# Performance work log

Hardware: AMD Instinct MI355X
Metric: run time of the kernel (lower is better)

The kernel has to match this reference:

```python
import jax, jax.numpy as jnp
import numpy as np


def setup_inputs() -> dict:
    key = jax.random.key(0)
    ks = jax.random.split(key, 5)
    N, C, H, W = 4, 256, 64, 64
    E, O = 256, 256  # embed_channels, out_channels
    scale = 1.0 / np.sqrt(C)
    return {
        "x": jax.random.normal(ks[0], (N, C, H, W), dtype=jnp.float32),
        "Wq": jax.random.normal(ks[1], (E, C), dtype=jnp.float32) * scale,
        "bq": jax.random.normal(ks[2], (E,), dtype=jnp.float32) * 0.01,
        "Wkv": jax.random.normal(ks[3], (E + O, C), dtype=jnp.float32) * scale,
        "bkv": jax.random.normal(ks[4], (E + O,), dtype=jnp.float32) * 0.01,
    }


def reference(x, Wq, bq, Wkv, bkv):
    n, c, h, w = x.shape
    E = Wq.shape[0]
    S = h * w
    # 1x1 convs == per-pixel linear projections over channels.
    # q: [n, S, E] (row-major hw flatten matches torch .view(n, C, -1))
    q = (jnp.einsum('nchw,ec->nhwe', x, Wq) + bq).reshape(n, S, E)
    kv = jnp.einsum('nchw,oc->nhwo', x, Wkv) + bkv  # [n, h, w, E+O]
    k = kv[..., :E].reshape(n, S, E)
    v = kv[..., E:].reshape(n, S, -1)  # [n, S, O]
    O = v.shape[-1]
    # Causal mask: tril with diagonal=0 (pixel may attend to itself and earlier).
    mask = jnp.tril(jnp.ones((S, S), dtype=bool))
    attn = jnp.einsum('nse,nte->nst', q, k) / np.sqrt(E)  # [n, S, S]
    attn = jnp.where(mask, attn, -jnp.inf)
    attn = jax.nn.softmax(attn, axis=-1)
    out = jnp.einsum('nst,nto->nso', attn, v)  # [n, S, O]
    return jnp.transpose(out, (0, 2, 1)).reshape(n, O, h, w)
```

## Files before the change

kernel.cpp:

```cpp
#include <hip/hip_runtime.h>
#include <hip/hip_bf16.h>

typedef __bf16 bf16x8 __attribute__((ext_vector_type(8)));
typedef float f32x4 __attribute__((ext_vector_type(4)));
typedef short short8 __attribute__((ext_vector_type(8)));
typedef short short4v __attribute__((ext_vector_type(4)));

#define NB 4
#define CC 256
#define SS 4096
#define EE 256

static constexpr float QSCALE = 1.4426950408889634f / 16.0f;

#define QOFF 0u
#define KOFF 8388608u
#define VOFF 16777216u
#define WOFF 25165824u
#define BOFF 25559040u
#define PAOFF 25690112u

#define GLOAD_LDS16(gsrc, ldst) \
    __builtin_amdgcn_global_load_lds((const __attribute__((address_space(1))) void*)(gsrc), \
                                     (__attribute__((address_space(3))) void*)(ldst), 16, 0, 0)

__global__ __launch_bounds__(256) void prep_kernel(const float* __restrict__ Wq,
                                                   const float* __restrict__ bq,
                                                   const float* __restrict__ Wkv,
                                                   const float* __restrict__ bkv,
                                                   __bf16* __restrict__ wc,
                                                   float* __restrict__ bias) {
    int r = blockIdx.x;
    int t = threadIdx.x;
    float v;
    if (r < 256) v = Wq[r * 256 + t] * QSCALE;
    else         v = Wkv[(r - 256) * 256 + t];
    wc[r * 256 + t] = (__bf16)v;
    if (t == 0) bias[r] = (r < 256) ? bq[r] * QSCALE : bkv[r - 256];
}

__global__ __launch_bounds__(256) void proj_kernel(const float* __restrict__ x,
                                                   const __bf16* __restrict__ wc,
                                                   const float* __restrict__ bias,
                                                   __bf16* __restrict__ qo,
                                                   __bf16* __restrict__ ko,
                                                   __bf16* __restrict__ vo) {
    __shared__ __align__(16) char Ab[32768];
    __shared__ __align__(16) char Wb[32768];
    const int t = threadIdx.x;
    const int lane = t & 63;
    const int w = t >> 6;
    const int n = blockIdx.x >> 6;
    const int s0 = (blockIdx.x & 63) << 6;

    {
        const int sl = t & 15;
        const int cc0 = t >> 4;
        #pragma unroll
        for (int it = 0; it < 2; ++it) {
            int c0 = (cc0 + (it << 4)) << 3;
            float f[8][4];
            #pragma unroll
            for (int r = 0; r < 8; ++r) {
                const float* xp = x + ((long)(n * CC + c0 + r)) * SS + s0 + sl;
                #pragma unroll
                for (int i = 0; i < 4; ++i) f[r][i] = xp[i << 4];
            }
            #pragma unroll
            for (int i = 0; i < 4; ++i) {
                bf16x8 v;
                #pragma unroll
                for (int r = 0; r < 8; ++r) v[r] = (__bf16)f[r][i];
                int srow = sl + (i << 4);
                *(bf16x8*)(Ab + srow * 512 + ((c0 * 2) ^ ((srow & 7) << 4))) = v;
            }
        }
    }
    __syncthreads();

    bf16x8 af[8];
    {
        int arow = (w << 4) + (lane & 15);
        #pragma unroll
        for (int kf = 0; kf < 8; ++kf) {
            int c = ((lane >> 4) << 3) + (kf << 5);
            af[kf] = *(const bf16x8*)(Ab + arow * 512 + ((c * 2) ^ ((arow & 7) << 4)));
        }
    }

    for (int ot = 0; ot < 12; ++ot) {
        #pragma unroll
        for (int p = 0; p < 16; ++p) {
            int row = w + (p << 2);
            int c = lane << 2;
            short4v vv = *(const short4v*)((const short*)wc + (ot * 64 + row) * 256 + c);
            *(short4v*)(Wb + row * 512 + ((c * 2) ^ ((row & 7) << 4))) = vv;
        }
        __syncthreads();

        f32x4 acc[4];
        #pragma unroll
        for (int cb = 0; cb < 4; ++cb) acc[cb] = (f32x4){0.f, 0.f, 0.f, 0.f};
        #pragma unroll
        for (int cb = 0; cb < 4; ++cb) {
            int row = (cb << 4) + (lane & 15);
            #pragma unroll
            for (int kf = 0; kf < 8; ++kf) {
                int c = ((lane >> 4) << 3) + (kf << 5);
                bf16x8 bfr = *(const bf16x8*)(Wb + row * 512 + ((c * 2) ^ ((row & 7) << 4)));
                acc[cb] = __builtin_amdgcn_mfma_f32_16x16x32_bf16(af[kf], bfr, acc[cb], 0, 0, 0);
            }
        }
        __syncthreads();

        __bf16* T = (__bf16*)Wb;
        float bsv[4];
        #pragma unroll
        for (int cb = 0; cb < 4; ++cb) bsv[cb] = bias[ot * 64 + (cb << 4) + (lane & 15)];

        if (ot < 8) {
            #pragma unroll
            for (int cb = 0; cb < 4; ++cb) {
                #pragma unroll
                for (int jj = 0; jj < 4; ++jj) {
                    int srow = (w << 4) + ((lane >> 4) << 2) + jj;
                    T[srow * 72 + (cb << 4) + (lane & 15)] = (__bf16)(acc[cb][jj] + bsv[cb]);
                }
            }
            __syncthreads();
            int s = t >> 2;
            int o0 = (t & 3) << 4;
            short8 r0 = *(const short8*)((const short*)T + s * 72 + o0);
            short8 r1 = *(const short8*)((const short*)T + s * 72 + o0 + 8);
            __bf16* dst = (ot < 4) ? qo : ko;
            long idx = ((long)(n * SS + s0 + s)) * EE + ((ot & 3) << 6) + o0;
            *(short8*)((short*)dst + idx) = r0;
            *(short8*)((short*)dst + idx + 8) = r1;
        } else {
            #pragma unroll
            for (int cb = 0; cb < 4; ++cb) {
                #pragma unroll
                for (int jj = 0; jj < 4; ++jj) {
                    int srow = (w << 4) + ((lane >> 4) << 2) + jj;
                    T[((cb << 4) + (lane & 15)) * 72 + srow] = (__bf16)(acc[cb][jj] + bsv[cb]);
                }
            }
            __syncthreads();
            int o = t >> 2;
            int sc0 = (t & 3) << 4;
            short8 r0 = *(const short8*)((const short*)T + o * 72 + sc0);
            short8 r1 = *(const short8*)((const short*)T + o * 72 + sc0 + 8);
            long idx = ((long)((n << 8) + ((ot - 8) << 6) + o)) * SS + s0 + sc0;
            *(short8*)((short*)vo + idx) = r0;
            *(short8*)((short*)vo + idx + 8) = r1;
        }
        __syncthreads();
    }
}

__global__ __launch_bounds__(512, 2) void attn_kernel(const __bf16* __restrict__ qg,
                                                      const __bf16* __restrict__ kg,
                                                      const __bf16* __restrict__ vg,
                                                      float* __restrict__ out,
                                                      float* __restrict__ pacc,
                                                      float2* __restrict__ pstats,
                                                      int chs, int ncs, int direct) {
    __shared__ __align__(16) char SMEM[147456];
    char* Pb = SMEM + 131072;
    const int t = threadIdx.x;
    const int lane = t & 63;
    const int w = t >> 6;

    const int b = blockIdx.x;
    const int c = b & ((1 << ncs) - 1);
    const int rest = b >> ncs;
    const int qtr = rest & 31;
    const int qt = 31 - qtr;
    const int n = rest >> 5;
    const int jtop = (qt << 1) + 1;
    const int jlo = c << chs;
    if (jlo > jtop) return;
    const int jhi = (jtop < jlo + (1 << chs) - 1) ? jtop : (jlo + (1 << chs) - 1);
    const int s0 = qt << 7;
    const int wr_direct = direct || ((jtop >> chs) == 0);

    auto stageK = [&](int j, int pb) {
        char* Kb = SMEM + (pb << 15);
        const int t0 = j << 6;
        #pragma unroll
        for (int i = 0; i < 4; ++i) {
            int rl = (i << 4) + (w << 1) + (lane >> 5);
            const short* src = (const short*)kg + ((long)(n * SS + t0 + rl)) * EE
                               + (((lane & 31) << 3) ^ ((rl & 7) << 3));
            GLOAD_LDS16(src, Kb + ((i << 4) + (w << 1)) * 512);
        }
    };
    auto stageV = [&](int j, int pb) {
        char* Vt = SMEM + 65536 + (pb << 15);
        const int t0 = j << 6;
        #pragma unroll
        for (int i = 0; i < 4; ++i) {
            int o = (i << 6) + (w << 3) + (lane >> 3);
            const short* src = (const short*)vg + ((long)((n << 8) + o)) * SS + t0
                               + (((lane & 7) << 3) ^ ((o & 7) << 3));
            GLOAD_LDS16(src, Vt + ((i << 6) + (w << 3)) * 128);
        }
    };

    bf16x8 qf[8];
    {
        int qrow = s0 + (w << 4) + (lane & 15);
        const short* qp = (const short*)qg + ((long)(n * SS + qrow)) * EE;
        #pragma unroll
        for (int kf = 0; kf < 8; ++kf)
            qf[kf] = *(const bf16x8*)(qp + ((lane >> 4) << 3) + (kf << 5));
    }

    float m_[4], ls[4];
    #pragma unroll
    for (int rr = 0; rr < 4; ++rr) { m_[rr] = -3e38f; ls[rr] = 0.f; }
    f32x4 acc[16];
    #pragma unroll
    for (int ocb = 0; ocb < 16; ++ocb) acc[ocb] = (f32x4){0.f, 0.f, 0.f, 0.f};

    stageK(jlo, jlo & 1);
    stageV(jlo, jlo & 1);

    for (int j = jlo; j <= jhi; ++j) {
        const int p = j & 1;
        const int t0 = j << 6;
        char* Kb = SMEM + (p << 15);
        char* Vt = SMEM + 65536 + (p << 15);
        __syncthreads();

        if (j < jhi) {
            stageK(j + 1, p ^ 1);
            stageV(j + 1, p ^ 1);
        }

        f32x4 sacc[4];
        #pragma unroll
        for (int cb = 0; cb < 4; ++cb) sacc[cb] = (f32x4){0.f, 0.f, 0.f, 0.f};
        #pragma unroll
        for (int cb = 0; cb < 4; ++cb) {
            int row = (cb << 4) + (lane & 15);
            #pragma unroll
            for (int kf = 0; kf < 8; ++kf) {
                int slot = (lane >> 4) + (kf << 2);
                bf16x8 kb = *(const bf16x8*)(Kb + row * 512 + ((slot ^ (row & 7)) << 4));
                sacc[cb] = __builtin_amdgcn_mfma_f32_16x16x32_bf16(qf[kf], kb, sacc[cb], 0, 0, 0);
            }
        }

        if ((j >> 1) == qt) {
            #pragma unroll
            for (int cb = 0; cb < 4; ++cb) {
                int key = t0 + (cb << 4) + (lane & 15);
                #pragma unroll
                for (int rr = 0; rr < 4; ++rr) {
                    int qr = s0 + (w << 4) + ((lane >> 4) << 2) + rr;
                    if (key > qr) sacc[cb][rr] = -1e30f;
                }
            }
        }

        float mx[4], ps[4], scl[4];
        #pragma unroll
        for (int rr = 0; rr < 4; ++rr)
            mx[rr] = fmaxf(fmaxf(sacc[0][rr], sacc[1][rr]), fmaxf(sacc[2][rr], sacc[3][rr]));
        #pragma unroll
        for (int off = 1; off < 16; off <<= 1) {
            #pragma unroll
            for (int rr = 0; rr < 4; ++rr) mx[rr] = fmaxf(mx[rr], __shfl_xor(mx[rr], off));
        }
        float pv[4][4];
        #pragma unroll
        for (int rr = 0; rr < 4; ++rr) {
            float mn = fmaxf(m_[rr], mx[rr]);
            scl[rr] = exp2f(m_[rr] - mn);
            m_[rr] = mn;
        }
        #pragma unroll
        for (int cb = 0; cb < 4; ++cb)
            #pragma unroll
            for (int rr = 0; rr < 4; ++rr) pv[cb][rr] = exp2f(sacc[cb][rr] - m_[rr]);
        #pragma unroll
        for (int rr = 0; rr < 4; ++rr)
            ps[rr] = (pv[0][rr] + pv[1][rr]) + (pv[2][rr] + pv[3][rr]);
        #pragma unroll
        for (int off = 1; off < 16; off <<= 1) {
            #pragma unroll
            for (int rr = 0; rr < 4; ++rr) ps[rr] += __shfl_xor(ps[rr], off);
        }
        #pragma unroll
        for (int rr = 0; rr < 4; ++rr) ls[rr] = ls[rr] * scl[rr] + ps[rr];

        #pragma unroll
        for (int cb = 0; cb < 4; ++cb)
            #pragma unroll
            for (int rr = 0; rr < 4; ++rr) {
                int row = ((lane >> 4) << 2) + rr;
                int col = (cb << 4) + (lane & 15);
                *(__bf16*)(Pb + (w << 11) + (row << 7)
                           + (((col >> 3) ^ (row & 7)) << 4) + ((col & 7) << 1)) = (__bf16)pv[cb][rr];
            }

        #pragma unroll
        for (int ocb = 0; ocb < 16; ++ocb)
            #pragma unroll
            for (int rr = 0; rr < 4; ++rr) acc[ocb][rr] *= scl[rr];

        bf16x8 pa[2];
        #pragma unroll
        for (int kf2 = 0; kf2 < 2; ++kf2) {
            int prow = lane & 15;
            int pslot = (lane >> 4) + (kf2 << 2);
            pa[kf2] = *(const bf16x8*)(Pb + (w << 11) + (prow << 7) + ((pslot ^ (prow & 7)) << 4));
        }
        #pragma unroll
        for (int ocb = 0; ocb < 16; ++ocb) {
            int orow = (ocb << 4) + (lane & 15);
            #pragma unroll
            for (int kf2 = 0; kf2 < 2; ++kf2) {
                int slot = (lane >> 4) + (kf2 << 2);
                bf16x8 vb = *(const bf16x8*)(Vt + (orow << 7) + ((slot ^ (orow & 7)) << 4));
                acc[ocb] = __builtin_amdgcn_mfma_f32_16x16x32_bf16(pa[kf2], vb, acc[ocb], 0, 0, 0);
            }
        }
    }

    if (!wr_direct && (lane & 15) == 0) {
        #pragma unroll
        for (int rr = 0; rr < 4; ++rr) {
            int s = (w << 4) + ((lane >> 4) << 2) + rr;
            pstats[(long)b * 128 + s] = make_float2(m_[rr], ls[rr]);
        }
    }

    float inv[4];
    #pragma unroll
    for (int rr = 0; rr < 4; ++rr) inv[rr] = wr_direct ? (1.0f / ls[rr]) : 1.0f;
    float* T = (float*)SMEM;

#define EPI_STAGE(g)                                                                    \
    do {                                                                                \
        __syncthreads();                                                                \
        _Pragma("unroll")                                                               \
        for (int e = 0; e < 2; ++e) {                                                   \
            _Pragma("unroll")                                                           \
            for (int rr = 0; rr < 4; ++rr) {                                            \
                int ol = (e << 4) + (lane & 15);                                        \
                int cl = (w << 4) + ((lane >> 4) << 2) + rr;                            \
                T[ol * 132 + cl] = acc[((g) << 1) + e][rr] * inv[rr];                   \
            }                                                                           \
        }                                                                               \
        __syncthreads();                                                                \
        {                                                                               \
            int row = t >> 4;                                                \
            int c0 = (t & 15) << 3;                               \
            float* dp = wr_direct                                                       \
                ? (out + ((long)((n << 8) + ((g) << 5) + row)) * SS + s0 + c0)          \
                : (pacc + ((long)b << 15) + ((((g) << 5) + row) << 7) + c0);            \
            f32x4 r0 = *(const f32x4*)(T + row * 132 + c0);                             \
            f32x4 r1 = *(const f32x4*)(T + row * 132 + c0 + 4);                         \
            *(f32x4*)dp = r0;                                                           \
            *(f32x4*)(dp + 4) = r1;                                                     \
        }                                                                               \
    } while (0)

    EPI_STAGE(0); EPI_STAGE(1); EPI_STAGE(2); EPI_STAGE(3);
    EPI_STAGE(4); EPI_STAGE(5); EPI_STAGE(6); EPI_STAGE(7);
#undef EPI_STAGE
}

__global__ __launch_bounds__(256) void combine_kernel(const float* __restrict__ pacc,
                                                      const float2* __restrict__ pstats,
                                                      float* __restrict__ out,
                                                      int chs, int ncs) {
    const int t = threadIdx.x;
    const int b2 = blockIdx.x;
    const int og = b2 & 7;
    const int qtr = (b2 >> 3) & 31;
    const int qt = 31 - qtr;
    const int n = b2 >> 8;
    const int jtop = (qt << 1) + 1;
    const int nch = (jtop >> chs) + 1;
    if (nch == 1) return;
    const long sb0 = (long)(((n << 5) + qtr) << ncs);

    __shared__ float wsc[8][128];
    __shared__ float invL[128];
    if (t < 128) {
        float M = -3e38f;
        for (int c2 = 0; c2 < nch; ++c2) M = fmaxf(M, pstats[(sb0 + c2) * 128 + t].x);
        float L = 0.f;
        for (int c2 = 0; c2 < nch; ++c2) {
            float2 st = pstats[(sb0 + c2) * 128 + t];
            float wv = exp2f(st.x - M);
            wsc[c2][t] = wv;
            L += st.y * wv;
        }
        invL[t] = 1.f / L;
    }
    __syncthreads();

    const int o = (og << 5) + (t >> 3);
    const int sc = (t & 7) << 4;
    float a[16];
    #pragma unroll
    for (int i = 0; i < 16; ++i) a[i] = 0.f;
    for (int c2 = 0; c2 < nch; ++c2) {
        const float* p = pacc + ((sb0 + c2) << 15) + (o << 7) + sc;
        #pragma unroll
        for (int u = 0; u < 4; ++u) {
            f32x4 v = *(const f32x4*)(p + (u << 2));
            #pragma unroll
            for (int k2 = 0; k2 < 4; ++k2) a[(u << 2) + k2] += v[k2] * wsc[c2][sc + (u << 2) + k2];
        }
    }
    float* op = out + ((long)((n << 8) + o)) * SS + (qt << 7) + sc;
    #pragma unroll
    for (int u = 0; u < 4; ++u) {
        f32x4 r;
        #pragma unroll
        for (int k2 = 0; k2 < 4; ++k2) r[k2] = a[(u << 2) + k2] * invL[sc + (u << 2) + k2];
        *(f32x4*)(op + (u << 2)) = r;
    }
}

extern "C" void kernel_launch(void* const* d_in, const int* in_sizes, int n_in,
                              void* d_out, int out_size, void* d_ws, size_t ws_size,
                              hipStream_t stream) {
    const float* x   = (const float*)d_in[0];
    const float* Wq  = (const float*)d_in[1];
    const float* bq  = (const float*)d_in[2];
    const float* Wkv = (const float*)d_in[3];
    const float* bkv = (const float*)d_in[4];
    float* out = (float*)d_out;
    char* ws = (char*)d_ws;
    __bf16* qw = (__bf16*)(ws + QOFF);
    __bf16* kw = (__bf16*)(ws + KOFF);
    __bf16* vw = (__bf16*)(ws + VOFF);
    __bf16* wc = (__bf16*)(ws + WOFF);
    float*  bias = (float*)(ws + BOFF);

    size_t need = (size_t)PAOFF + (size_t)1024 * 131072 + (size_t)1024 * 1024;
    int direct = (ws_size < need) ? 1 : 0;
    int ncs = direct ? 0 : 3;
    int chs = direct ? 6 : 3;
    float* pacc = (float*)(ws + PAOFF);
    float2* pstats = (float2*)(ws + PAOFF + (size_t)1024 * 131072);

    prep_kernel<<<dim3(768), dim3(256), 0, stream>>>(Wq, bq, Wkv, bkv, wc, bias);
    proj_kernel<<<dim3(256), dim3(256), 0, stream>>>(x, wc, bias, qw, kw, vw);
    attn_kernel<<<dim3(128 << ncs), dim3(512), 0, stream>>>(qw, kw, vw, out, pacc, pstats,
                                                            chs, ncs, direct);
    if (!direct)
        combine_kernel<<<dim3(1024), dim3(256), 0, stream>>>(pacc, pstats, out, chs, ncs);
}
```

Before: 199.1 us.

## Remap attention blocks to XCDs per batch and skip unneeded softmax rescales

Block IDs are remapped so that each pair of XCDs handles a single batch element, so its K/V tiles stay in that XCD's L2. The partial-output and stats slots are indexed to match the new mapping. Separately, the online softmax now keeps the running max unchanged when every row's new max exceeds it by at most 8 (log2 units), which skips the exp2 and the 64-register accumulator rescale on most iterations. The deferred max allows exponentials up to 2^8, a small overflow and precision risk in bf16 P. It also adds a wave-wide vote each iteration.

```diff
diff --git a/kernel.cpp b/kernel.cpp
--- a/kernel.cpp
+++ b/kernel.cpp
@@ -171,12 +171,13 @@
     const int lane = t & 63;
     const int w = t >> 6;
 
-    const int b = blockIdx.x;
-    const int c = b & ((1 << ncs) - 1);
-    const int rest = b >> ncs;
-    const int qtr = rest & 31;
+    const int xcd = blockIdx.x & 7;
+    const int n = xcd >> 1;
+    const int id = ((blockIdx.x >> 3) << 1) | (xcd & 1);
+    const int c = id & ((1 << ncs) - 1);
+    const int qtr = (id >> ncs) & 31;
     const int qt = 31 - qtr;
-    const int n = rest >> 5;
+    const long slot = ((long)n << (5 + ncs)) + id;
     const int jtop = (qt << 1) + 1;
     const int jlo = c << chs;
     if (jlo > jtop) return;
@@ -246,8 +247,8 @@
             int row = (cb << 4) + (lane & 15);
             #pragma unroll
             for (int kf = 0; kf < 8; ++kf) {
-                int slot = (lane >> 4) + (kf << 2);
-                bf16x8 kb = *(const bf16x8*)(Kb + row * 512 + ((slot ^ (row & 7)) << 4));
+                int slotk = (lane >> 4) + (kf << 2);
+                bf16x8 kb = *(const bf16x8*)(Kb + row * 512 + ((slotk ^ (row & 7)) << 4));
                 sacc[cb] = __builtin_amdgcn_mfma_f32_16x16x32_bf16(qf[kf], kb, sacc[cb], 0, 0, 0);
             }
         }
@@ -273,13 +274,22 @@
             #pragma unroll
             for (int rr = 0; rr < 4; ++rr) mx[rr] = fmaxf(mx[rr], __shfl_xor(mx[rr], off));
         }
+        bool okd = true;
+        #pragma unroll
+        for (int rr = 0; rr < 4; ++rr) okd = okd && (mx[rr] - m_[rr] <= 8.0f);
+        const bool need_rescale = !__all(okd);
+        if (need_rescale) {
+            #pragma unroll
+            for (int rr = 0; rr < 4; ++rr) {
+                float mn = fmaxf(m_[rr], mx[rr]);
+                scl[rr] = exp2f(m_[rr] - mn);
+                m_[rr] = mn;
+            }
+        } else {
+            #pragma unroll
+            for (int rr = 0; rr < 4; ++rr) scl[rr] = 1.0f;
+        }
         float pv[4][4];
-        #pragma unroll
-        for (int rr = 0; rr < 4; ++rr) {
-            float mn = fmaxf(m_[rr], mx[rr]);
-            scl[rr] = exp2f(m_[rr] - mn);
-            m_[rr] = mn;
-        }
         #pragma unroll
         for (int cb = 0; cb < 4; ++cb)
             #pragma unroll
@@ -305,10 +315,12 @@
                            + (((col >> 3) ^ (row & 7)) << 4) + ((col & 7) << 1)) = (__bf16)pv[cb][rr];
             }
 
-        #pragma unroll
-        for (int ocb = 0; ocb < 16; ++ocb)
-            #pragma unroll
-            for (int rr = 0; rr < 4; ++rr) acc[ocb][rr] *= scl[rr];
+        if (need_rescale) {
+            #pragma unroll
+            for (int ocb = 0; ocb < 16; ++ocb)
+                #pragma unroll
+                for (int rr = 0; rr < 4; ++rr) acc[ocb][rr] *= scl[rr];
+        }
 
         bf16x8 pa[2];
         #pragma unroll
@@ -322,8 +334,8 @@
             int orow = (ocb << 4) + (lane & 15);
             #pragma unroll
             for (int kf2 = 0; kf2 < 2; ++kf2) {
-                int slot = (lane >> 4) + (kf2 << 2);
-                bf16x8 vb = *(const bf16x8*)(Vt + (orow << 7) + ((slot ^ (orow & 7)) << 4));
+                int slotv = (lane >> 4) + (kf2 << 2);
+                bf16x8 vb = *(const bf16x8*)(Vt + (orow << 7) + ((slotv ^ (orow & 7)) << 4));
                 acc[ocb] = __builtin_amdgcn_mfma_f32_16x16x32_bf16(pa[kf2], vb, acc[ocb], 0, 0, 0);
             }
         }
@@ -333,7 +345,7 @@
         #pragma unroll
         for (int rr = 0; rr < 4; ++rr) {
             int s = (w << 4) + ((lane >> 4) << 2) + rr;
-            pstats[(long)b * 128 + s] = make_float2(m_[rr], ls[rr]);
+            pstats[slot * 128 + s] = make_float2(m_[rr], ls[rr]);
         }
     }
 
@@ -360,7 +372,7 @@
             int c0 = (t & 15) << 3;                               \
             float* dp = wr_direct                                                       \
                 ? (out + ((long)((n << 8) + ((g) << 5) + row)) * SS + s0 + c0)          \
-                : (pacc + ((long)b << 15) + ((((g) << 5) + row) << 7) + c0);            \
+                : (pacc + (slot << 15) + ((((g) << 5) + row) << 7) + c0);               \
             f32x4 r0 = *(const f32x4*)(T + row * 132 + c0);                             \
             f32x4 r1 = *(const f32x4*)(T + row * 132 + c0 + 4);                         \
             *(f32x4*)dp = r0;                                                           \
```

Result: faster. 194.6 us (-2.3%).
